# Optimization experiments

Hardware: AMD Instinct MI355X
Metric: run time of the kernel (lower is better)

Reference implementation:

```python
import jax, jax.numpy as jnp
import numpy as np

N_SUPPORT = 4096
N_QUERY = 8192
H = W = 28
IN_DIM = H * W  # 784
EMBED_DIM = 512
N_CLASSES = 64


def setup_inputs() -> dict:
    key = jax.random.key(0)
    k1, k2, k3, k4 = jax.random.split(key, 4)
    support_set = jax.random.normal(k1, (N_SUPPORT, 1, H, W), dtype=jnp.float32)
    query_set = jax.random.normal(k2, (N_QUERY, 1, H, W), dtype=jnp.float32)
    # one-hot support labels (N, C)
    lbl = jax.random.randint(k3, (N_SUPPORT,), 0, N_CLASSES)
    support_labels = jax.nn.one_hot(lbl, N_CLASSES, dtype=jnp.float32)
    # encoder params: flatten + dense projection stand-in for embedding_net
    W_enc = jax.random.normal(k4, (IN_DIM, EMBED_DIM), dtype=jnp.float32) * (1.0 / np.sqrt(IN_DIM))
    b_enc = jnp.zeros((EMBED_DIM,), dtype=jnp.float32)
    return {
        "support_set": support_set,
        "query_set": query_set,
        "support_labels": support_labels,
        "W_enc": W_enc,
        "b_enc": b_enc,
    }


def _encode(x, W_enc, b_enc):
    # (B, 1, H, W) -> (B, D): flatten + linear projection
    B = x.shape[0]
    return x.reshape(B, -1) @ W_enc + b_enc


def _neg_cdist(q, s):
    # -euclidean distance, computed via the expansion ||q-s||^2 = |q|^2 + |s|^2 - 2 q.s
    q2 = jnp.sum(q * q, axis=-1, keepdims=True)          # (Q, 1)
    s2 = jnp.sum(s * s, axis=-1)[None, :]                # (1, N)
    qs = jnp.einsum("qd,nd->qn", q, s)                  # (Q, N)
    d2 = jnp.maximum(q2 + s2 - 2.0 * qs, 0.0)
    return -jnp.sqrt(d2)


def reference(support_set, query_set, support_labels, W_enc, b_enc):
    support_emb = _encode(support_set, W_enc, b_enc)     # (N, D)
    query_emb = _encode(query_set, W_enc, b_enc)         # (Q, D)
    distances = _neg_cdist(query_emb, support_emb)       # (Q, N)
    attention = jax.nn.softmax(distances, axis=1)        # (Q, N)
    predictions = attention @ support_labels             # (Q, C)
    return predictions
```

## Files before the change

### kernel.cpp

```cpp
#include <hip/hip_runtime.h>

#define N_SUP 4096
#define N_QRY 8192
#define IN_DIM 784
#define EMB 512
#define NCLS 64
#define M_TOT (N_SUP + N_QRY)
#define NCHUNK 25
#define XCH 13

typedef _Float16 f16;
typedef _Float16 f16x8 __attribute__((ext_vector_type(8)));
typedef float f32x4 __attribute__((ext_vector_type(4)));

static __device__ __forceinline__ f16x8 cvt8(const float* p) {
    float4 a = *(const float4*)p;
    float4 b = *(const float4*)(p + 4);
    f16x8 v;
    v[0] = (f16)a.x; v[1] = (f16)a.y; v[2] = (f16)a.z; v[3] = (f16)a.w;
    v[4] = (f16)b.x; v[5] = (f16)b.y; v[6] = (f16)b.z; v[7] = (f16)b.w;
    return v;
}

__global__ __launch_bounds__(256) void prep_wb(const float* __restrict__ W,
                                               f16* __restrict__ Wb) {
    int g = blockIdx.x * 256 + threadIdx.x;
    if (g >= NCHUNK * 32 * 64) return;
    int chunk = g >> 11;
    int rem = g & 2047;
    int nbg = rem >> 6, lane = rem & 63;
    int n = nbg * 16 + (lane & 15);
    int kbase = chunk * 32 + (lane >> 4) * 8;
    f16x8 v;
#pragma unroll
    for (int j = 0; j < 8; ++j) {
        int k = kbase + j;
        v[j] = (k < IN_DIM) ? (f16)W[(size_t)k * EMB + n] : (f16)0.f;
    }
    *(f16x8*)(Wb + (size_t)g * 8) = v;
}

__global__ __launch_bounds__(256) void prep_lbl(const float* __restrict__ lab,
                                                int* __restrict__ lbl) {
    const int w = threadIdx.x >> 6, lane = threadIdx.x & 63;
    const int s = blockIdx.x * 4 + w;
    float v = lab[(size_t)s * NCLS + lane];
    int c = lane;
#pragma unroll
    for (int off = 1; off < 64; off <<= 1) {
        float v2 = __shfl_xor(v, off);
        int c2 = __shfl_xor(c, off);
        if (v2 > v || (v2 == v && c2 < c)) { v = v2; c = c2; }
    }
    if (lane == 0) lbl[s] = c;
}

__global__ __launch_bounds__(256) void prep_L(const int* __restrict__ lbl,
                                              f16* __restrict__ Lcs) {
    int idx = blockIdx.x * 256 + threadIdx.x;
    if (idx >= NCLS * N_SUP) return;
    int c = idx >> 12, s = idx & (N_SUP - 1);
    Lcs[idx] = (lbl[s] == c) ? (f16)1.f : (f16)0.f;
}

__global__ __launch_bounds__(256) void encode(
    const float* __restrict__ sup, const float* __restrict__ qry,
    const f16* __restrict__ Wb, const float* __restrict__ bias,
    f16* __restrict__ E, float* __restrict__ norms)
{
    __shared__ __align__(16) f16 Xs[32][72];
    const int tid = threadIdx.x;
    const int w = tid >> 6, lane = tid & 63;
    const int q = lane >> 4, c16 = lane & 15;
    const int mb = blockIdx.x >> 1;
    const int ch = blockIdx.x & 1;
    const int m0 = mb * 32;
    const int rbase = (w & 1) * 16;
    const int nbg0 = ch * 16 + (w >> 1) * 8;
    const int cbase = nbg0 * 16;

    f32x4 acc[8];
#pragma unroll
    for (int nb = 0; nb < 8; ++nb) acc[nb] = (f32x4){0.f, 0.f, 0.f, 0.f};

    const int sr = tid >> 3;
    const int sq = tid & 7;
    const float* xrow;
    {
        int gr = m0 + sr;
        xrow = (gr < N_SUP) ? sup + (size_t)gr * IN_DIM
                            : qry + (size_t)(gr - N_SUP) * IN_DIM;
    }

    f16x8 xg = cvt8(xrow + sq * 8);

    for (int c = 0; c < XCH; ++c) {
        __syncthreads();
        *(f16x8*)&Xs[sr][sq * 8] = xg;
        __syncthreads();
        if (c + 1 < XCH) {
            int k = (c + 1) * 64 + sq * 8;
            xg = (k + 8 <= IN_DIM) ? cvt8(xrow + k) : (f16x8){0,0,0,0,0,0,0,0};
        }
#pragma unroll
        for (int kc = 0; kc < 2; ++kc) {
            int c32 = c * 2 + kc;
            if (c32 >= NCHUNK) break;
            f16x8 a = *(const f16x8*)&Xs[rbase + c16][kc * 32 + q * 8];
            const f16* wb = Wb + ((size_t)(c32 * 32 + nbg0) * 64 + lane) * 8;
#pragma unroll
            for (int nb = 0; nb < 8; ++nb) {
                f16x8 b = *(const f16x8*)(wb + (size_t)nb * 512);
                acc[nb] = __builtin_amdgcn_mfma_f32_16x16x32_f16(a, b, acc[nb], 0, 0, 0);
            }
        }
    }

    float nrm[4] = {0.f, 0.f, 0.f, 0.f};
#pragma unroll
    for (int nb = 0; nb < 8; ++nb) {
        int col = cbase + nb * 16 + c16;
        float bv = bias[col];
#pragma unroll
        for (int r = 0; r < 4; ++r) {
            int row = m0 + rbase + q * 4 + r;
            float v = acc[nb][r] + bv;
            E[(size_t)row * EMB + col] = (f16)v;
            nrm[r] += v * v;
        }
    }
#pragma unroll
    for (int r = 0; r < 4; ++r) {
        float v = nrm[r];
        v += __shfl_xor(v, 1); v += __shfl_xor(v, 2);
        v += __shfl_xor(v, 4); v += __shfl_xor(v, 8);
        if (c16 == 0) atomicAdd(&norms[m0 + rbase + q * 4 + r], v);
    }
}

__global__ __launch_bounds__(256) void anchor(const f16* __restrict__ E,
                                              const float* __restrict__ norms,
                                              float* __restrict__ manc) {
    const int w = threadIdx.x >> 6, lane = threadIdx.x & 63;
    const int qrow = blockIdx.x * 4 + w;
    f16x8 qv = *(const f16x8*)(E + (size_t)(N_SUP + qrow) * EMB + lane * 8);
    f16x8 sv = *(const f16x8*)(E + lane * 8);
    float dot = 0.f;
#pragma unroll
    for (int j = 0; j < 8; ++j) dot += (float)qv[j] * (float)sv[j];
    dot += __shfl_xor(dot, 1);  dot += __shfl_xor(dot, 2);
    dot += __shfl_xor(dot, 4);  dot += __shfl_xor(dot, 8);
    dot += __shfl_xor(dot, 16); dot += __shfl_xor(dot, 32);
    if (lane == 0) {
        float d2 = fmaxf(norms[N_SUP + qrow] + norms[0] - 2.f * dot, 0.f);
        manc[qrow] = sqrtf(d2);
    }
}

__global__ __launch_bounds__(256, 3) void attn(
    const f16* __restrict__ E, const float* __restrict__ norms,
    const float* __restrict__ manc, const f16* __restrict__ Lcs,
    float* __restrict__ Num)
{
    __shared__ __align__(16) f16 Ss[2][64][144];
    __shared__ __align__(16) f16 Pt[4][16][80];
    const int tid = threadIdx.x;
    const int w = tid >> 6, lane = tid & 63;
    const int q = lane >> 4, c16 = lane & 15;
    const int ss = blockIdx.x & 7;
    const int qt = blockIdx.x >> 3;

    f16x8 qf[16];
    const f16* qb = E + (size_t)(N_SUP + qt * 64 + w * 16 + c16) * EMB + q * 8;
#pragma unroll
    for (int ks = 0; ks < 16; ++ks) qf[ks] = *(const f16x8*)(qb + ks * 32);
    float q2[4], mrow[4];
#pragma unroll
    for (int r = 0; r < 4; ++r) {
        q2[r]   = norms[N_SUP + qt * 64 + w * 16 + q * 4 + r];
        mrow[r] = manc[qt * 64 + w * 16 + q * 4 + r];
    }

    f32x4 accPL[4];
#pragma unroll
    for (int nb = 0; nb < 4; ++nb) accPL[nb] = (f32x4){0.f, 0.f, 0.f, 0.f};

    const int sr = tid >> 2, koff0 = (tid & 3) * 8;
    const f16* sbase = E + (size_t)(ss * 512 + sr) * EMB;

    f16x8 g[4];
#pragma unroll
    for (int i = 0; i < 4; ++i) g[i] = *(const f16x8*)(sbase + koff0 + i * 32);
#pragma unroll
    for (int i = 0; i < 4; ++i) *(f16x8*)&Ss[0][sr][koff0 + i * 32] = g[i];
    __syncthreads();

    for (int it = 0; it < 8; ++it) {
        f32x4 accQK[4];
#pragma unroll
        for (int nb = 0; nb < 4; ++nb) accQK[nb] = (f32x4){0.f, 0.f, 0.f, 0.f};
#pragma unroll
        for (int kc = 0; kc < 4; ++kc) {
            const int idx = it * 4 + kc;
            const int cur = idx & 1;
            if (idx + 1 < 32) {
                const int nit = (idx + 1) >> 2, nkc = (idx + 1) & 3;
                const f16* src = sbase + (size_t)(nit * 64) * EMB + nkc * 128 + koff0;
#pragma unroll
                for (int i = 0; i < 4; ++i) g[i] = *(const f16x8*)(src + i * 32);
            }
#pragma unroll
            for (int ksl = 0; ksl < 4; ++ksl) {
#pragma unroll
                for (int nb = 0; nb < 4; ++nb) {
                    f16x8 b = *(const f16x8*)&Ss[cur][nb * 16 + c16][ksl * 32 + q * 8];
                    accQK[nb] = __builtin_amdgcn_mfma_f32_16x16x32_f16(qf[kc * 4 + ksl], b, accQK[nb], 0, 0, 0);
                }
            }
            if (idx + 1 < 32) {
#pragma unroll
                for (int i = 0; i < 4; ++i) *(f16x8*)&Ss[cur ^ 1][sr][koff0 + i * 32] = g[i];
            }
            __syncthreads();
        }
        const int s0g = ss * 512 + it * 64;
#pragma unroll
        for (int nb = 0; nb < 4; ++nb) {
            const int col = s0g + nb * 16 + c16;
            const float s2 = norms[col];
#pragma unroll
            for (int r = 0; r < 4; ++r) {
                float d2 = fmaxf(q2[r] + s2 - 2.f * accQK[nb][r], 0.f);
                float p = __expf(mrow[r] - sqrtf(d2));
                p = fminf(p, 60000.f);
                Pt[w][q * 4 + r][nb * 16 + c16] = (f16)p;
            }
        }
#pragma unroll
        for (int kc2 = 0; kc2 < 2; ++kc2) {
            f16x8 af = *(const f16x8*)&Pt[w][c16][kc2 * 32 + q * 8];
#pragma unroll
            for (int nbc = 0; nbc < 4; ++nbc) {
                f16x8 bl = *(const f16x8*)(Lcs + (size_t)(nbc * 16 + c16) * N_SUP + s0g + kc2 * 32 + q * 8);
                accPL[nbc] = __builtin_amdgcn_mfma_f32_16x16x32_f16(af, bl, accPL[nbc], 0, 0, 0);
            }
        }
    }
#pragma unroll
    for (int nbc = 0; nbc < 4; ++nbc)
#pragma unroll
        for (int r = 0; r < 4; ++r)
            atomicAdd(&Num[(size_t)(qt * 64 + w * 16 + q * 4 + r) * NCLS + nbc * 16 + c16],
                      accPL[nbc][r]);
}

__global__ __launch_bounds__(256) void finalize(const float* __restrict__ Num,
                                                float* __restrict__ out) {
    const int tid = threadIdx.x;
    const int w = tid >> 6, lane = tid & 63;
    const int qrow = blockIdx.x * 4 + w;
    float v = Num[(size_t)qrow * NCLS + lane];
    float s = v;
    s += __shfl_xor(s, 1);  s += __shfl_xor(s, 2);  s += __shfl_xor(s, 4);
    s += __shfl_xor(s, 8);  s += __shfl_xor(s, 16); s += __shfl_xor(s, 32);
    out[(size_t)qrow * NCLS + lane] = v / s;
}

extern "C" void kernel_launch(void* const* d_in, const int* in_sizes, int n_in,
                              void* d_out, int out_size, void* d_ws, size_t ws_size,
                              hipStream_t stream) {
    (void)in_sizes; (void)n_in; (void)out_size; (void)ws_size;
    const float* sup  = (const float*)d_in[0];
    const float* qry  = (const float*)d_in[1];
    const float* lab  = (const float*)d_in[2];
    const float* Wenc = (const float*)d_in[3];
    const float* benc = (const float*)d_in[4];
    float* out = (float*)d_out;

    char* ws = (char*)d_ws;
    size_t off = 0;
    f16* Wb = (f16*)(ws + off);        off += (size_t)NCHUNK * 32 * 64 * 8 * 2;
    f16* E  = (f16*)(ws + off);        off += (size_t)M_TOT * EMB * 2;
    int* lbl = (int*)(ws + off);       off += (size_t)N_SUP * 4;
    f16* Lcs = (f16*)(ws + off);       off += (size_t)NCLS * N_SUP * 2;
    float* manc = (float*)(ws + off);  off += (size_t)N_QRY * 4;
    float* norms = (float*)(ws + off); off += (size_t)M_TOT * 4;
    float* Num = (float*)(ws + off);   off += (size_t)N_QRY * NCLS * 4;

    hipMemsetAsync(norms, 0, (size_t)M_TOT * 4 + (size_t)N_QRY * NCLS * 4, stream);

    prep_wb<<<(NCHUNK * 32 * 64 + 255) / 256, 256, 0, stream>>>(Wenc, Wb);
    prep_lbl<<<N_SUP / 4, 256, 0, stream>>>(lab, lbl);
    prep_L<<<NCLS * N_SUP / 256, 256, 0, stream>>>(lbl, Lcs);
    encode<<<M_TOT / 32 * 2, 256, 0, stream>>>(sup, qry, Wb, benc, E, norms);
    anchor<<<N_QRY / 4, 256, 0, stream>>>(E, norms, manc);
    attn<<<N_QRY / 64 * 8, 256, 0, stream>>>(E, norms, manc, Lcs, Num);
    finalize<<<N_QRY / 4, 256, 0, stream>>>(Num, out);
}
```

Baseline: 218.4 us.

## Stream XOR-swizzled support tiles into LDS with direct global-to-LDS loads

Adds a prep kernel that writes support embeddings into a row-wise XOR-swizzled layout. The attention kernel then loads whole 32-row by 512-dim support tiles straight into double-buffered LDS with global_load_lds, dropping the register staging and the per-k-chunk barriers. The loop is restructured to 16 tiles of 32 supports, with one sync per tile and label fragments prefetched early. The larger LDS footprint lowers occupancy to 2 blocks per CU, and the extra prep kernel adds launch and memory traffic.

Result: faster. 197.8 us (-9.4%).

```diff
diff --git a/kernel.cpp b/kernel.cpp
--- a/kernel.cpp
+++ b/kernel.cpp
@@ -12,6 +12,11 @@
 typedef _Float16 f16;
 typedef _Float16 f16x8 __attribute__((ext_vector_type(8)));
 typedef float f32x4 __attribute__((ext_vector_type(4)));
+
+#define GLDS16(gp, lp)                                                        \
+    __builtin_amdgcn_global_load_lds(                                         \
+        (const __attribute__((address_space(1))) void*)(gp),                  \
+        (__attribute__((address_space(3))) void*)(lp), 16, 0, 0)
 
 static __device__ __forceinline__ f16x8 cvt8(const float* p) {
     float4 a = *(const float4*)p;
@@ -61,6 +66,14 @@
     if (idx >= NCLS * N_SUP) return;
     int c = idx >> 12, s = idx & (N_SUP - 1);
     Lcs[idx] = (lbl[s] == c) ? (f16)1.f : (f16)0.f;
+}
+
+__global__ __launch_bounds__(256) void prep_sb(const f16* __restrict__ E,
+                                               f16* __restrict__ Sb) {
+    int g = blockIdx.x * 256 + threadIdx.x;
+    int s = g >> 6, lg = g & 63;
+    f16x8 v = *(const f16x8*)(E + (size_t)s * EMB + lg * 8);
+    *(f16x8*)(Sb + (size_t)s * EMB + ((lg ^ (s & 15)) * 8)) = v;
 }
 
 __global__ __launch_bounds__(256) void encode(
@@ -157,13 +170,13 @@
     }
 }
 
-__global__ __launch_bounds__(256, 3) void attn(
+__global__ __launch_bounds__(256, 2) void attn(
     const f16* __restrict__ E, const float* __restrict__ norms,
     const float* __restrict__ manc, const f16* __restrict__ Lcs,
-    float* __restrict__ Num)
+    const f16* __restrict__ Sb, float* __restrict__ Num)
 {
-    __shared__ __align__(16) f16 Ss[2][64][144];
-    __shared__ __align__(16) f16 Pt[4][16][80];
+    __shared__ __align__(16) f16 Ss[2][32 * EMB];
+    __shared__ __align__(16) f16 Pt[4][16][40];
     const int tid = threadIdx.x;
     const int w = tid >> 6, lane = tid & 63;
     const int q = lane >> 4, c16 = lane & 15;
@@ -185,47 +198,49 @@
 #pragma unroll
     for (int nb = 0; nb < 4; ++nb) accPL[nb] = (f32x4){0.f, 0.f, 0.f, 0.f};
 
-    const int sr = tid >> 2, koff0 = (tid & 3) * 8;
-    const f16* sbase = E + (size_t)(ss * 512 + sr) * EMB;
-
-    f16x8 g[4];
-#pragma unroll
-    for (int i = 0; i < 4; ++i) g[i] = *(const f16x8*)(sbase + koff0 + i * 32);
-#pragma unroll
-    for (int i = 0; i < 4; ++i) *(f16x8*)&Ss[0][sr][koff0 + i * 32] = g[i];
+    const f16* sb_base = Sb + (size_t)(ss * 512) * EMB;
+    const int wslot = w * 512;
+
+#pragma unroll
+    for (int i = 0; i < 8; ++i)
+        GLDS16(sb_base + (size_t)(wslot + i * 64 + lane) * 8,
+               &Ss[0][(wslot + i * 64) * 8]);
     __syncthreads();
 
-    for (int it = 0; it < 8; ++it) {
-        f32x4 accQK[4];
-#pragma unroll
-        for (int nb = 0; nb < 4; ++nb) accQK[nb] = (f32x4){0.f, 0.f, 0.f, 0.f};
+    for (int t = 0; t < 16; ++t) {
+        const int cur = t & 1;
+        if (t + 1 < 16) {
+            const f16* gsrc = sb_base + (size_t)(t + 1) * 32 * EMB;
+#pragma unroll
+            for (int i = 0; i < 8; ++i)
+                GLDS16(gsrc + (size_t)(wslot + i * 64 + lane) * 8,
+                       &Ss[cur ^ 1][(wslot + i * 64) * 8]);
+        }
+        const int s0g = ss * 512 + t * 32;
+        f16x8 bl[4];
+#pragma unroll
+        for (int nbc = 0; nbc < 4; ++nbc)
+            bl[nbc] = *(const f16x8*)(Lcs + (size_t)(nbc * 16 + c16) * N_SUP + s0g + q * 8);
+
+        f32x4 accQK[2];
+        accQK[0] = (f32x4){0.f, 0.f, 0.f, 0.f};
+        accQK[1] = (f32x4){0.f, 0.f, 0.f, 0.f};
 #pragma unroll
         for (int kc = 0; kc < 4; ++kc) {
-            const int idx = it * 4 + kc;
-            const int cur = idx & 1;
-            if (idx + 1 < 32) {
-                const int nit = (idx + 1) >> 2, nkc = (idx + 1) & 3;
-                const f16* src = sbase + (size_t)(nit * 64) * EMB + nkc * 128 + koff0;
-#pragma unroll
-                for (int i = 0; i < 4; ++i) g[i] = *(const f16x8*)(src + i * 32);
-            }
 #pragma unroll
             for (int ksl = 0; ksl < 4; ++ksl) {
-#pragma unroll
-                for (int nb = 0; nb < 4; ++nb) {
-                    f16x8 b = *(const f16x8*)&Ss[cur][nb * 16 + c16][ksl * 32 + q * 8];
-                    accQK[nb] = __builtin_amdgcn_mfma_f32_16x16x32_f16(qf[kc * 4 + ksl], b, accQK[nb], 0, 0, 0);
+                const int lg = kc * 16 + ksl * 4 + q;
+#pragma unroll
+                for (int nb = 0; nb < 2; ++nb) {
+                    const int r = nb * 16 + c16;
+                    f16x8 b = *(const f16x8*)&Ss[cur][r * EMB + ((lg ^ c16) * 8)];
+                    accQK[nb] = __builtin_amdgcn_mfma_f32_16x16x32_f16(
+                        qf[kc * 4 + ksl], b, accQK[nb], 0, 0, 0);
                 }
             }
-            if (idx + 1 < 32) {
-#pragma unroll
-                for (int i = 0; i < 4; ++i) *(f16x8*)&Ss[cur ^ 1][sr][koff0 + i * 32] = g[i];
-            }
-            __syncthreads();
-        }
-        const int s0g = ss * 512 + it * 64;
-#pragma unroll
-        for (int nb = 0; nb < 4; ++nb) {
+        }
+#pragma unroll
+        for (int nb = 0; nb < 2; ++nb) {
             const int col = s0g + nb * 16 + c16;
             const float s2 = norms[col];
 #pragma unroll
@@ -236,16 +251,14 @@
                 Pt[w][q * 4 + r][nb * 16 + c16] = (f16)p;
             }
         }
-#pragma unroll
-        for (int kc2 = 0; kc2 < 2; ++kc2) {
-            f16x8 af = *(const f16x8*)&Pt[w][c16][kc2 * 32 + q * 8];
-#pragma unroll
-            for (int nbc = 0; nbc < 4; ++nbc) {
-                f16x8 bl = *(const f16x8*)(Lcs + (size_t)(nbc * 16 + c16) * N_SUP + s0g + kc2 * 32 + q * 8);
-                accPL[nbc] = __builtin_amdgcn_mfma_f32_16x16x32_f16(af, bl, accPL[nbc], 0, 0, 0);
-            }
-        }
-    }
+        f16x8 af = *(const f16x8*)&Pt[w][c16][q * 8];
+#pragma unroll
+        for (int nbc = 0; nbc < 4; ++nbc)
+            accPL[nbc] = __builtin_amdgcn_mfma_f32_16x16x32_f16(af, bl[nbc], accPL[nbc], 0, 0, 0);
+
+        __syncthreads();
+    }
+
 #pragma unroll
     for (int nbc = 0; nbc < 4; ++nbc)
 #pragma unroll
@@ -281,6 +294,7 @@
     size_t off = 0;
     f16* Wb = (f16*)(ws + off);        off += (size_t)NCHUNK * 32 * 64 * 8 * 2;
     f16* E  = (f16*)(ws + off);        off += (size_t)M_TOT * EMB * 2;
+    f16* Sb = (f16*)(ws + off);        off += (size_t)N_SUP * EMB * 2;
     int* lbl = (int*)(ws + off);       off += (size_t)N_SUP * 4;
     f16* Lcs = (f16*)(ws + off);       off += (size_t)NCLS * N_SUP * 2;
     float* manc = (float*)(ws + off);  off += (size_t)N_QRY * 4;
@@ -293,7 +307,8 @@
     prep_lbl<<<N_SUP / 4, 256, 0, stream>>>(lab, lbl);
     prep_L<<<NCLS * N_SUP / 256, 256, 0, stream>>>(lbl, Lcs);
     encode<<<M_TOT / 32 * 2, 256, 0, stream>>>(sup, qry, Wb, benc, E, norms);
+    prep_sb<<<N_SUP * 64 / 256, 256, 0, stream>>>(E, Sb);
     anchor<<<N_QRY / 4, 256, 0, stream>>>(E, norms, manc);
-    attn<<<N_QRY / 64 * 8, 256, 0, stream>>>(E, norms, manc, Lcs, Num);
+    attn<<<N_QRY / 64 * 8, 256, 0, stream>>>(E, norms, manc, Lcs, Sb, Num);
     finalize<<<N_QRY / 4, 256, 0, stream>>>(Num, out);
 }
```
